# Kernel optimization log

Hardware: AMD Instinct MI355X
Metric: run time of the kernel (lower is better)

The kernel has to match this reference:

```python
import jax, jax.numpy as jnp
import numpy as np

B_SZ, C_IN, H, W = 2, 96, 128, 128
DT_RANK, D_STATE, D_INNER = 8, 16, 96


def pscan2d(A, X):
    """Faithful port of PScan2DUnified.forward / pscan2d_optimized.

    A, X: (b, H, W, d, N). The source's downsweep writes into index_select
    COPIES (discarded in torch), so the effective computation is the upsweep
    only: at level k (stride s=2**k), for each 2x2 block of active elements,
    X[dst] += A[dst] * X[src]; A[dst] *= A[src], where src=(s-1::2s, s-1::2s)
    and dst=(2s-1::2s, 2s-1::2s). Requires H, W powers of two.
    """
    h, w = A.shape[1], A.shape[2]
    K = min(int(np.log2(h)), int(np.log2(w)))
    for k in range(K):
        s = 2 ** k
        Asrc = A[:, s - 1::2 * s, s - 1::2 * s]
        Xsrc = X[:, s - 1::2 * s, s - 1::2 * s]
        Adst = A[:, 2 * s - 1::2 * s, 2 * s - 1::2 * s]
        X = X.at[:, 2 * s - 1::2 * s, 2 * s - 1::2 * s].add(Adst * Xsrc)
        A = A.at[:, 2 * s - 1::2 * s, 2 * s - 1::2 * s].multiply(Asrc)
    return X


def setup_inputs() -> dict:
    key = jax.random.key(0)
    ks = jax.random.split(key, 5)
    x = jax.random.normal(ks[0], (B_SZ, C_IN, H, W), dtype=jnp.float32)
    # 1x1 conv weights stored as (out, in) matrices
    deltaBC_w = jax.random.normal(ks[1], (DT_RANK + 2 * D_STATE, C_IN), dtype=jnp.float32) * 0.02
    deltaBC_b = jnp.zeros((DT_RANK + 2 * D_STATE,), dtype=jnp.float32)
    dt_w = jax.random.normal(ks[2], (D_INNER, DT_RANK), dtype=jnp.float32) * 0.02
    dt_b = jnp.zeros((D_INNER,), dtype=jnp.float32)
    # faithful init: log(linspace(1,2,N)) repeated over d_inner
    A_log = jnp.tile(jnp.log(jnp.linspace(1.0, 2.0, D_STATE, dtype=jnp.float32)), (D_INNER, 1))
    D = jnp.ones((D_INNER,), dtype=jnp.float32)
    return {"x": x, "deltaBC_w": deltaBC_w, "deltaBC_b": deltaBC_b,
            "dt_w": dt_w, "dt_b": dt_b, "A_log": A_log, "D": D}


def reference(x, deltaBC_w, deltaBC_b, dt_w, dt_b, A_log, D):
    A = -jnp.exp(A_log)  # (d, N)
    # 1x1 conv == per-pixel matmul
    dBC = jnp.einsum('bchw,oc->bohw', x, deltaBC_w) + deltaBC_b[None, :, None, None]
    delta = dBC[:, :DT_RANK]
    Bm = dBC[:, DT_RANK:DT_RANK + D_STATE]
    Cm = dBC[:, DT_RANK + D_STATE:]
    delta = jax.nn.softplus(jnp.einsum('bchw,oc->bohw', delta, dt_w) + dt_b[None, :, None, None])
    delta = delta.transpose(0, 2, 3, 1)   # (b,H,W,d)
    Bm = Bm.transpose(0, 2, 3, 1)         # (b,H,W,N)
    Cm = Cm.transpose(0, 2, 3, 1)         # (b,H,W,N)
    xh = x.transpose(0, 2, 3, 1)          # (b,H,W,d)
    A_bar = jnp.exp(delta[..., None] * A)                         # (b,H,W,d,N)
    BX = (delta[..., None] * Bm[:, :, :, None, :]) * xh[..., None]  # (b,H,W,d,N)
    hs = pscan2d(A_bar, BX)                                       # (b,H,W,d,N)
    y = jnp.einsum('bhwdn,bhwn->bhwd', hs, Cm) + D * xh
    return y
```

## Files before the change

### kernel.cpp

```cpp
#include <hip/hip_runtime.h>
#include <cstdint>

#define CIN 96
#define DIN 96
#define DTR 8
#define DST 16
#define HH 128
#define WW 128
#define HW (HH*WW)
#define NPIX (2*HW)
#define DIAG (WW+1)
#define SHORT_BLOCKS 2048
#define LONG_BLOCKS 512

__device__ __forceinline__ float softplus_f(float t) {
    return (t > 20.0f) ? t : __logf(1.0f + __expf(t));
}

__global__ __launch_bounds__(512) void ssm2d_dbc(
    const float* __restrict__ x,
    const float* __restrict__ W1, const float* __restrict__ b1,
    const float* __restrict__ dtw, const float* __restrict__ dtb,
    const float* __restrict__ alog, const float* __restrict__ Dv,
    float* __restrict__ bc, float2* __restrict__ dc,
    float* __restrict__ Aws, float* __restrict__ out)
{
    __shared__ float sX[CIN][65];
    __shared__ float sOut[64][41];
    __shared__ float sBC[64];

    const int t = threadIdx.x;
    const int p0 = blockIdx.x * 64;
    const int bb = p0 >> 14;
    const int q0 = p0 & (HW - 1);
    const float* xb = x + (size_t)bb * CIN * HW + q0;

    #pragma unroll
    for (int it = 0; it < 3; ++it) {
        int i = it * 512 + t;
        int ch = i >> 4;
        int p4 = (i & 15) << 2;
        float4 v = *reinterpret_cast<const float4*>(xb + (size_t)ch * HW + p4);
        sX[ch][p4 + 0] = v.x; sX[ch][p4 + 1] = v.y;
        sX[ch][p4 + 2] = v.z; sX[ch][p4 + 3] = v.w;
    }
    if (blockIdx.x == 0) {
        for (int i = t; i < DIN * DST; i += 512) {
            int d = i >> 4, n = i & 15;
            Aws[n * DIN + d] = -__expf(alog[i]);
        }
    }
    __syncthreads();

    const int lane = t & 63;
    const int w = __builtin_amdgcn_readfirstlane(t >> 6);
    const int og = w * 5;

    float a0 = b1[og + 0], a1 = b1[og + 1], a2 = b1[og + 2],
          a3 = b1[og + 3], a4 = b1[og + 4];
    #pragma unroll 16
    for (int ch = 0; ch < CIN; ++ch) {
        float xv = sX[ch][lane];
        a0 = fmaf(xv, W1[(og + 0) * CIN + ch], a0);
        a1 = fmaf(xv, W1[(og + 1) * CIN + ch], a1);
        a2 = fmaf(xv, W1[(og + 2) * CIN + ch], a2);
        a3 = fmaf(xv, W1[(og + 3) * CIN + ch], a3);
        a4 = fmaf(xv, W1[(og + 4) * CIN + ch], a4);
    }
    sOut[lane][og + 0] = a0; sOut[lane][og + 1] = a1; sOut[lane][og + 2] = a2;
    sOut[lane][og + 3] = a3; sOut[lane][og + 4] = a4;
    __syncthreads();

    if (t < 64) {
        float s = 0.f;
        #pragma unroll
        for (int n = 0; n < DST; ++n) s += sOut[t][8 + n] * sOut[t][24 + n];
        sBC[t] = s;
    }
    __syncthreads();

    #pragma unroll
    for (int it = 0; it < 12; ++it) {
        int i = it * 512 + t;
        int px = i / 96;
        int d = i - px * 96;
        float tt = dtb[d];
        float4 wA = *reinterpret_cast<const float4*>(dtw + d * DTR);
        float4 wB = *reinterpret_cast<const float4*>(dtw + d * DTR + 4);
        tt = fmaf(sOut[px][0], wA.x, tt); tt = fmaf(sOut[px][1], wA.y, tt);
        tt = fmaf(sOut[px][2], wA.z, tt); tt = fmaf(sOut[px][3], wA.w, tt);
        tt = fmaf(sOut[px][4], wB.x, tt); tt = fmaf(sOut[px][5], wB.y, tt);
        tt = fmaf(sOut[px][6], wB.z, tt); tt = fmaf(sOut[px][7], wB.w, tt);
        float delta = softplus_f(tt);
        float xv = sX[d][px];
        out[(size_t)p0 * 96 + i] = xv * fmaf(delta, sBC[px], Dv[d]);
        dc[(size_t)p0 * 96 + i] = make_float2(delta, delta * xv);
    }

    {
        int px = t >> 3;
        int o4 = (t & 7) << 2;
        float4 v = make_float4(sOut[px][8 + o4], sOut[px][9 + o4],
                               sOut[px][10 + o4], sOut[px][11 + o4]);
        *reinterpret_cast<float4*>(bc + (size_t)(p0 + px) * 32 + o4) = v;
    }
}

__global__ __launch_bounds__(384) void ssm2d_scan(
    const float* __restrict__ bc, const float2* __restrict__ dc,
    const float* __restrict__ Aws, float* __restrict__ out)
{
    const int t = threadIdx.x;
    if (blockIdx.x < SHORT_BLOCKS) {
        const int lp = t / DIN;
        const int d = t - lp * DIN;
        const int pix = blockIdx.x * 4 + lp;
        const int b = pix >> 12;
        const int rem = pix & 4095;
        const int r = ((rem >> 6) << 1) + 1;
        const int c = ((rem & 63) << 1) + 1;
        const int p = b * HW + r * WW + c;
        int m = __builtin_ctz(r + 1);
        int mc = __builtin_ctz(c + 1);
        if (mc < m) m = mc;
        if (m >= 5) return;
        const int L = 1 << m;

        float An[16];
        #pragma unroll
        for (int n = 0; n < 16; ++n) An[n] = Aws[n * DIN + d];
        float acc16[16];
        #pragma unroll
        for (int n = 0; n < 16; ++n) acc16[n] = 0.f;

        float S = dc[(size_t)p * 96 + d].x;
        int pj = p;
        for (int j = 1; j < L; ++j) {
            pj -= DIAG;
            float2 v = dc[(size_t)pj * 96 + d];
            float cj = v.y;
            const float* rb = bc + (size_t)pj * 32;
            float4 B0 = *reinterpret_cast<const float4*>(rb);
            float4 B1 = *reinterpret_cast<const float4*>(rb + 4);
            float4 B2 = *reinterpret_cast<const float4*>(rb + 8);
            float4 B3 = *reinterpret_cast<const float4*>(rb + 12);
            float Bv[16] = {B0.x,B0.y,B0.z,B0.w, B1.x,B1.y,B1.z,B1.w,
                            B2.x,B2.y,B2.z,B2.w, B3.x,B3.y,B3.z,B3.w};
            #pragma unroll
            for (int n = 0; n < 16; ++n)
                acc16[n] = fmaf(__expf(An[n] * S) * Bv[n], cj, acc16[n]);
            S += v.x;
        }
        const float* rc = bc + (size_t)p * 32 + 16;
        float4 C0 = *reinterpret_cast<const float4*>(rc);
        float4 C1 = *reinterpret_cast<const float4*>(rc + 4);
        float4 C2 = *reinterpret_cast<const float4*>(rc + 8);
        float4 C3 = *reinterpret_cast<const float4*>(rc + 12);
        float ys = 0.f;
        ys = fmaf(acc16[0],C0.x,ys); ys = fmaf(acc16[1],C0.y,ys);
        ys = fmaf(acc16[2],C0.z,ys); ys = fmaf(acc16[3],C0.w,ys);
        ys = fmaf(acc16[4],C1.x,ys); ys = fmaf(acc16[5],C1.y,ys);
        ys = fmaf(acc16[6],C1.z,ys); ys = fmaf(acc16[7],C1.w,ys);
        ys = fmaf(acc16[8],C2.x,ys); ys = fmaf(acc16[9],C2.y,ys);
        ys = fmaf(acc16[10],C2.z,ys); ys = fmaf(acc16[11],C2.w,ys);
        ys = fmaf(acc16[12],C3.x,ys); ys = fmaf(acc16[13],C3.y,ys);
        ys = fmaf(acc16[14],C3.z,ys); ys = fmaf(acc16[15],C3.w,ys);
        out[(size_t)p * 96 + d] += ys;
    } else {
        const int wv = t >> 6;
        const int lane = t & 63;
        int waveid = (blockIdx.x - SHORT_BLOCKS) * 6 + wv;
        int pix = waveid / DIN;
        int d = waveid - pix * DIN;
        int batch = pix >> 4;
        int sel = pix & 15;
        int r = ((sel >> 2) + 1) * 32 - 1;
        int c = ((sel & 3) + 1) * 32 - 1;
        int p = batch * HW + r * WW + c;
        int m = __builtin_ctz(r + 1);
        int mc = __builtin_ctz(c + 1);
        if (mc < m) m = mc;
        int L = 1 << m;

        float An[16];
        #pragma unroll
        for (int n = 0; n < 16; ++n) An[n] = Aws[n * DIN + d];

        float acc16[16];
        #pragma unroll
        for (int n = 0; n < 16; ++n) acc16[n] = 0.0f;
        float Scarry = 0.0f;

        for (int jb = 0; jb < L; jb += 64) {
            int j = jb + lane;
            bool act = (j < L);
            int jc = act ? j : 0;
            int pj = p - DIAG * jc;
            float2 v = dc[(size_t)pj * 96 + d];
            float dj = act ? v.x : 0.0f;
            float cj = (j >= 1 && act) ? v.y : 0.0f;

            float incl = dj;
            #pragma unroll
            for (int off = 1; off < 64; off <<= 1) {
                float u = __shfl_up(incl, off);
                if (lane >= off) incl += u;
            }
            float S = Scarry + incl - dj;

            const float* rb = bc + (size_t)pj * 32;
            float4 B0 = *reinterpret_cast<const float4*>(rb);
            float4 B1 = *reinterpret_cast<const float4*>(rb + 4);
            float4 B2 = *reinterpret_cast<const float4*>(rb + 8);
            float4 B3 = *reinterpret_cast<const float4*>(rb + 12);
            float Bv[16] = {B0.x,B0.y,B0.z,B0.w, B1.x,B1.y,B1.z,B1.w,
                            B2.x,B2.y,B2.z,B2.w, B3.x,B3.y,B3.z,B3.w};
            #pragma unroll
            for (int n = 0; n < 16; ++n)
                acc16[n] = fmaf(__expf(An[n] * S) * Bv[n], cj, acc16[n]);

            Scarry += __shfl(incl, 63);
        }

        #pragma unroll
        for (int off = 32; off >= 1; off >>= 1) {
            #pragma unroll
            for (int n = 0; n < 16; ++n) acc16[n] += __shfl_xor(acc16[n], off);
        }

        if (lane == 0) {
            const float* rc = bc + (size_t)p * 32 + 16;
            float4 C0 = *reinterpret_cast<const float4*>(rc);
            float4 C1 = *reinterpret_cast<const float4*>(rc + 4);
            float4 C2 = *reinterpret_cast<const float4*>(rc + 8);
            float4 C3 = *reinterpret_cast<const float4*>(rc + 12);
            float y = 0.0f;
            y = fmaf(acc16[0],C0.x,y); y = fmaf(acc16[1],C0.y,y);
            y = fmaf(acc16[2],C0.z,y); y = fmaf(acc16[3],C0.w,y);
            y = fmaf(acc16[4],C1.x,y); y = fmaf(acc16[5],C1.y,y);
            y = fmaf(acc16[6],C1.z,y); y = fmaf(acc16[7],C1.w,y);
            y = fmaf(acc16[8],C2.x,y); y = fmaf(acc16[9],C2.y,y);
            y = fmaf(acc16[10],C2.z,y); y = fmaf(acc16[11],C2.w,y);
            y = fmaf(acc16[12],C3.x,y); y = fmaf(acc16[13],C3.y,y);
            y = fmaf(acc16[14],C3.z,y); y = fmaf(acc16[15],C3.w,y);
            out[(size_t)p * 96 + d] += y;
        }
    }
}

extern "C" void kernel_launch(void* const* d_in, const int* in_sizes, int n_in,
                              void* d_out, int out_size, void* d_ws, size_t ws_size,
                              hipStream_t stream) {
    const float* x    = (const float*)d_in[0];
    const float* W1   = (const float*)d_in[1];
    const float* b1   = (const float*)d_in[2];
    const float* dtw  = (const float*)d_in[3];
    const float* dtb  = (const float*)d_in[4];
    const float* alog = (const float*)d_in[5];
    const float* Dv   = (const float*)d_in[6];
    float* out = (float*)d_out;

    char* ws = (char*)d_ws;
    float2* dc  = (float2*)(ws);
    float*  bcb = (float*)(ws + 25165824);
    float*  Aws = (float*)(ws + 29360128);

    hipLaunchKernelGGL(ssm2d_dbc, dim3(NPIX / 64), dim3(512), 0, stream,
                       x, W1, b1, dtw, dtb, alog, Dv,
                       bcb, dc, Aws, out);
    hipLaunchKernelGGL(ssm2d_scan, dim3(SHORT_BLOCKS + LONG_BLOCKS), dim3(384), 0, stream,
                       bcb, dc, Aws, out);
}
```

Before: 46.18 us.

## Split short scan chains into per-length block ranges with templated unrolled loops

The short-chain scan region is split into four block ranges, one per chain length (2, 4, 8, 16). Each block now handles only pixels of one length, which removes intra-block divergence and the early-exit threads, and the two shortest lengths use fully unrolled templated loops with loads issued up front. The A matrix is stored transposed (d-major) with log2(e) folded in, so it loads as float4s and exp2f replaces __expf. More blocks are launched, and the branch selection and index math grow slightly more complex.

```diff
diff --git a/kernel.cpp b/kernel.cpp
--- a/kernel.cpp
+++ b/kernel.cpp
@@ -10,11 +10,112 @@
 #define HW (HH*WW)
 #define NPIX (2*HW)
 #define DIAG (WW+1)
-#define SHORT_BLOCKS 2048
+#define LOG2E 1.4426950408889634f
+
+#define M1_BLOCKS 2048
+#define M2_BLOCKS 512
+#define M3_BLOCKS 128
+#define M4_BLOCKS 32
 #define LONG_BLOCKS 512
+#define SCAN_BLOCKS (M1_BLOCKS + M2_BLOCKS + M3_BLOCKS + M4_BLOCKS + LONG_BLOCKS)
 
 __device__ __forceinline__ float softplus_f(float t) {
     return (t > 20.0f) ? t : __logf(1.0f + __expf(t));
+}
+
+__device__ __forceinline__ void load_An(const float* __restrict__ AwsT, int d, float* An) {
+    float4 A0 = *reinterpret_cast<const float4*>(AwsT + d * 16);
+    float4 A1 = *reinterpret_cast<const float4*>(AwsT + d * 16 + 4);
+    float4 A2 = *reinterpret_cast<const float4*>(AwsT + d * 16 + 8);
+    float4 A3 = *reinterpret_cast<const float4*>(AwsT + d * 16 + 12);
+    An[0]=A0.x; An[1]=A0.y; An[2]=A0.z; An[3]=A0.w;
+    An[4]=A1.x; An[5]=A1.y; An[6]=A1.z; An[7]=A1.w;
+    An[8]=A2.x; An[9]=A2.y; An[10]=A2.z; An[11]=A2.w;
+    An[12]=A3.x; An[13]=A3.y; An[14]=A3.z; An[15]=A3.w;
+}
+
+__device__ __forceinline__ float c_dot(const float* __restrict__ rc, const float* acc16) {
+    float4 C0 = *reinterpret_cast<const float4*>(rc);
+    float4 C1 = *reinterpret_cast<const float4*>(rc + 4);
+    float4 C2 = *reinterpret_cast<const float4*>(rc + 8);
+    float4 C3 = *reinterpret_cast<const float4*>(rc + 12);
+    float ys = 0.f;
+    ys = fmaf(acc16[0],C0.x,ys); ys = fmaf(acc16[1],C0.y,ys);
+    ys = fmaf(acc16[2],C0.z,ys); ys = fmaf(acc16[3],C0.w,ys);
+    ys = fmaf(acc16[4],C1.x,ys); ys = fmaf(acc16[5],C1.y,ys);
+    ys = fmaf(acc16[6],C1.z,ys); ys = fmaf(acc16[7],C1.w,ys);
+    ys = fmaf(acc16[8],C2.x,ys); ys = fmaf(acc16[9],C2.y,ys);
+    ys = fmaf(acc16[10],C2.z,ys); ys = fmaf(acc16[11],C2.w,ys);
+    ys = fmaf(acc16[12],C3.x,ys); ys = fmaf(acc16[13],C3.y,ys);
+    ys = fmaf(acc16[14],C3.z,ys); ys = fmaf(acc16[15],C3.w,ys);
+    return ys;
+}
+
+template<int L>
+__device__ __forceinline__ void chain_LT(int p, int d,
+    const float* __restrict__ bc, const float2* __restrict__ dc,
+    const float* __restrict__ AwsT, float* __restrict__ out)
+{
+    size_t base = (size_t)p * 96 + d;
+    float ybase = out[base];
+    float2 v0 = dc[base];
+    float2 vj[L - 1];
+    #pragma unroll
+    for (int j = 1; j < L; ++j)
+        vj[j - 1] = dc[(size_t)(p - j * DIAG) * 96 + d];
+    float An[16];
+    load_An(AwsT, d, An);
+    float acc16[16];
+    #pragma unroll
+    for (int n = 0; n < 16; ++n) acc16[n] = 0.f;
+    float S = v0.x;
+    #pragma unroll
+    for (int j = 1; j < L; ++j) {
+        const float* rb = bc + (size_t)(p - j * DIAG) * 32;
+        float4 B0 = *reinterpret_cast<const float4*>(rb);
+        float4 B1 = *reinterpret_cast<const float4*>(rb + 4);
+        float4 B2 = *reinterpret_cast<const float4*>(rb + 8);
+        float4 B3 = *reinterpret_cast<const float4*>(rb + 12);
+        float Bv[16] = {B0.x,B0.y,B0.z,B0.w, B1.x,B1.y,B1.z,B1.w,
+                        B2.x,B2.y,B2.z,B2.w, B3.x,B3.y,B3.z,B3.w};
+        float cj = vj[j - 1].y;
+        #pragma unroll
+        for (int n = 0; n < 16; ++n)
+            acc16[n] = fmaf(exp2f(An[n] * S) * Bv[n], cj, acc16[n]);
+        S += vj[j - 1].x;
+    }
+    out[base] = ybase + c_dot(bc + (size_t)p * 32 + 16, acc16);
+}
+
+__device__ __forceinline__ void chain_RT(int p, int d, int L,
+    const float* __restrict__ bc, const float2* __restrict__ dc,
+    const float* __restrict__ AwsT, float* __restrict__ out)
+{
+    size_t base = (size_t)p * 96 + d;
+    float ybase = out[base];
+    float An[16];
+    load_An(AwsT, d, An);
+    float acc16[16];
+    #pragma unroll
+    for (int n = 0; n < 16; ++n) acc16[n] = 0.f;
+    float S = dc[base].x;
+    int pj = p;
+    for (int j = 1; j < L; ++j) {
+        pj -= DIAG;
+        float2 v = dc[(size_t)pj * 96 + d];
+        const float* rb = bc + (size_t)pj * 32;
+        float4 B0 = *reinterpret_cast<const float4*>(rb);
+        float4 B1 = *reinterpret_cast<const float4*>(rb + 4);
+        float4 B2 = *reinterpret_cast<const float4*>(rb + 8);
+        float4 B3 = *reinterpret_cast<const float4*>(rb + 12);
+        float Bv[16] = {B0.x,B0.y,B0.z,B0.w, B1.x,B1.y,B1.z,B1.w,
+                        B2.x,B2.y,B2.z,B2.w, B3.x,B3.y,B3.z,B3.w};
+        #pragma unroll
+        for (int n = 0; n < 16; ++n)
+            acc16[n] = fmaf(exp2f(An[n] * S) * Bv[n], v.y, acc16[n]);
+        S += v.x;
+    }
+    out[base] = ybase + c_dot(bc + (size_t)p * 32 + 16, acc16);
 }
 
 __global__ __launch_bounds__(512) void ssm2d_dbc(
@@ -45,10 +146,8 @@
         sX[ch][p4 + 2] = v.z; sX[ch][p4 + 3] = v.w;
     }
     if (blockIdx.x == 0) {
-        for (int i = t; i < DIN * DST; i += 512) {
-            int d = i >> 4, n = i & 15;
-            Aws[n * DIN + d] = -__expf(alog[i]);
-        }
+        for (int i = t; i < DIN * DST; i += 512)
+            Aws[i] = -__expf(alog[i]) * LOG2E;
     }
     __syncthreads();
 
@@ -108,68 +207,37 @@
 
 __global__ __launch_bounds__(384) void ssm2d_scan(
     const float* __restrict__ bc, const float2* __restrict__ dc,
-    const float* __restrict__ Aws, float* __restrict__ out)
+    const float* __restrict__ AwsT, float* __restrict__ out)
 {
     const int t = threadIdx.x;
-    if (blockIdx.x < SHORT_BLOCKS) {
+    const int blk = blockIdx.x;
+    if (blk < M1_BLOCKS + M2_BLOCKS + M3_BLOCKS + M4_BLOCKS) {
+        int M, base;
+        if (blk < M1_BLOCKS)                          { M = 1; base = 0; }
+        else if (blk < M1_BLOCKS + M2_BLOCKS)         { M = 2; base = M1_BLOCKS; }
+        else if (blk < M1_BLOCKS + M2_BLOCKS + M3_BLOCKS) { M = 3; base = M1_BLOCKS + M2_BLOCKS; }
+        else                                          { M = 4; base = M1_BLOCKS + M2_BLOCKS + M3_BLOCKS; }
         const int lp = t / DIN;
         const int d = t - lp * DIN;
-        const int pix = blockIdx.x * 4 + lp;
-        const int b = pix >> 12;
-        const int rem = pix & 4095;
-        const int r = ((rem >> 6) << 1) + 1;
-        const int c = ((rem & 63) << 1) + 1;
-        const int p = b * HW + r * WW + c;
-        int m = __builtin_ctz(r + 1);
-        int mc = __builtin_ctz(c + 1);
-        if (mc < m) m = mc;
-        if (m >= 5) return;
-        const int L = 1 << m;
-
-        float An[16];
-        #pragma unroll
-        for (int n = 0; n < 16; ++n) An[n] = Aws[n * DIN + d];
-        float acc16[16];
-        #pragma unroll
-        for (int n = 0; n < 16; ++n) acc16[n] = 0.f;
-
-        float S = dc[(size_t)p * 96 + d].x;
-        int pj = p;
-        for (int j = 1; j < L; ++j) {
-            pj -= DIAG;
-            float2 v = dc[(size_t)pj * 96 + d];
-            float cj = v.y;
-            const float* rb = bc + (size_t)pj * 32;
-            float4 B0 = *reinterpret_cast<const float4*>(rb);
-            float4 B1 = *reinterpret_cast<const float4*>(rb + 4);
-            float4 B2 = *reinterpret_cast<const float4*>(rb + 8);
-            float4 B3 = *reinterpret_cast<const float4*>(rb + 12);
-            float Bv[16] = {B0.x,B0.y,B0.z,B0.w, B1.x,B1.y,B1.z,B1.w,
-                            B2.x,B2.y,B2.z,B2.w, B3.x,B3.y,B3.z,B3.w};
-            #pragma unroll
-            for (int n = 0; n < 16; ++n)
-                acc16[n] = fmaf(__expf(An[n] * S) * Bv[n], cj, acc16[n]);
-            S += v.x;
-        }
-        const float* rc = bc + (size_t)p * 32 + 16;
-        float4 C0 = *reinterpret_cast<const float4*>(rc);
-        float4 C1 = *reinterpret_cast<const float4*>(rc + 4);
-        float4 C2 = *reinterpret_cast<const float4*>(rc + 8);
-        float4 C3 = *reinterpret_cast<const float4*>(rc + 12);
-        float ys = 0.f;
-        ys = fmaf(acc16[0],C0.x,ys); ys = fmaf(acc16[1],C0.y,ys);
-        ys = fmaf(acc16[2],C0.z,ys); ys = fmaf(acc16[3],C0.w,ys);
-        ys = fmaf(acc16[4],C1.x,ys); ys = fmaf(acc16[5],C1.y,ys);
-        ys = fmaf(acc16[6],C1.z,ys); ys = fmaf(acc16[7],C1.w,ys);
-        ys = fmaf(acc16[8],C2.x,ys); ys = fmaf(acc16[9],C2.y,ys);
-        ys = fmaf(acc16[10],C2.z,ys); ys = fmaf(acc16[11],C2.w,ys);
-        ys = fmaf(acc16[12],C3.x,ys); ys = fmaf(acc16[13],C3.y,ys);
-        ys = fmaf(acc16[14],C3.z,ys); ys = fmaf(acc16[15],C3.w,ys);
-        out[(size_t)p * 96 + d] += ys;
+        int idx = (blk - base) * 4 + lp;
+        int nM = 128 >> M;
+        int half = nM * nM;
+        int img = idx >= half;
+        int e = idx - img * half;
+        int rr = e >> (7 - M);
+        int cc = e & (nM - 1);
+        if (((rr & cc) & 1) != 0) return;
+        int r = ((rr + 1) << M) - 1;
+        int cx = ((cc + 1) << M) - 1;
+        int p = img * HW + r * WW + cx;
+        if (M == 1)      chain_LT<2>(p, d, bc, dc, AwsT, out);
+        else if (M == 2) chain_LT<4>(p, d, bc, dc, AwsT, out);
+        else if (M == 3) chain_RT(p, d, 8, bc, dc, AwsT, out);
+        else             chain_RT(p, d, 16, bc, dc, AwsT, out);
     } else {
         const int wv = t >> 6;
         const int lane = t & 63;
-        int waveid = (blockIdx.x - SHORT_BLOCKS) * 6 + wv;
+        int waveid = (blk - (M1_BLOCKS + M2_BLOCKS + M3_BLOCKS + M4_BLOCKS)) * 6 + wv;
         int pix = waveid / DIN;
         int d = waveid - pix * DIN;
         int batch = pix >> 4;
@@ -183,8 +251,7 @@
         int L = 1 << m;
 
         float An[16];
-        #pragma unroll
-        for (int n = 0; n < 16; ++n) An[n] = Aws[n * DIN + d];
+        load_An(AwsT, d, An);
 
         float acc16[16];
         #pragma unroll
@@ -217,7 +284,7 @@
                             B2.x,B2.y,B2.z,B2.w, B3.x,B3.y,B3.z,B3.w};
             #pragma unroll
             for (int n = 0; n < 16; ++n)
-                acc16[n] = fmaf(__expf(An[n] * S) * Bv[n], cj, acc16[n]);
+                acc16[n] = fmaf(exp2f(An[n] * S) * Bv[n], cj, acc16[n]);
 
             Scarry += __shfl(incl, 63);
         }
@@ -229,20 +296,7 @@
         }
 
         if (lane == 0) {
-            const float* rc = bc + (size_t)p * 32 + 16;
-            float4 C0 = *reinterpret_cast<const float4*>(rc);
-            float4 C1 = *reinterpret_cast<const float4*>(rc + 4);
-            float4 C2 = *reinterpret_cast<const float4*>(rc + 8);
-            float4 C3 = *reinterpret_cast<const float4*>(rc + 12);
-            float y = 0.0f;
-            y = fmaf(acc16[0],C0.x,y); y = fmaf(acc16[1],C0.y,y);
-            y = fmaf(acc16[2],C0.z,y); y = fmaf(acc16[3],C0.w,y);
-            y = fmaf(acc16[4],C1.x,y); y = fmaf(acc16[5],C1.y,y);
-            y = fmaf(acc16[6],C1.z,y); y = fmaf(acc16[7],C1.w,y);
-            y = fmaf(acc16[8],C2.x,y); y = fmaf(acc16[9],C2.y,y);
-            y = fmaf(acc16[10],C2.z,y); y = fmaf(acc16[11],C2.w,y);
-            y = fmaf(acc16[12],C3.x,y); y = fmaf(acc16[13],C3.y,y);
-            y = fmaf(acc16[14],C3.z,y); y = fmaf(acc16[15],C3.w,y);
+            float y = c_dot(bc + (size_t)p * 32 + 16, acc16);
             out[(size_t)p * 96 + d] += y;
         }
     }
@@ -268,6 +322,6 @@
     hipLaunchKernelGGL(ssm2d_dbc, dim3(NPIX / 64), dim3(512), 0, stream,
                        x, W1, b1, dtw, dtb, alog, Dv,
                        bcb, dc, Aws, out);
-    hipLaunchKernelGGL(ssm2d_scan, dim3(SHORT_BLOCKS + LONG_BLOCKS), dim3(384), 0, stream,
+    hipLaunchKernelGGL(ssm2d_scan, dim3(SCAN_BLOCKS), dim3(384), 0, stream,
                        bcb, dc, Aws, out);
 }
```

Measured after the change: 47.79 us. +3.5%, slower.

## Replace per-pixel scan with per-diagonal LDS-staged prefix-sum kernel

Applied to the files above, without the earlier changes.

The scan stage is restructured so each block handles one anti-diagonal of one batch. It stages delta (recomputed from stored dt-rank projections), delta*x, B and C into LDS, then builds prefix sums of delta along the diagonal so each segment sum becomes a difference of two prefix values. This removes the repeated global gathers and per-wave shuffle scans of the old short/long split, and halves the dc workspace by storing only delta*x plus the 8-wide rank vector. The exp is folded into exp2 with a pre-scaled A, laid out d-major for float4 loads. The new grid is only 254 blocks with heavy LDS use (~110KB per block) and uneven diagonal lengths, so occupancy and load balance become risks.

```diff
diff --git a/kernel.cpp b/kernel.cpp
--- a/kernel.cpp
+++ b/kernel.cpp
@@ -10,11 +10,21 @@
 #define HW (HH*WW)
 #define NPIX (2*HW)
 #define DIAG (WW+1)
-#define SHORT_BLOCKS 2048
-#define LONG_BLOCKS 512
+#define LOG2E 1.4426950408889634f
 
 __device__ __forceinline__ float softplus_f(float t) {
     return (t > 20.0f) ? t : __logf(1.0f + __expf(t));
+}
+
+__device__ __forceinline__ void load_An(const float* __restrict__ AwsT, int d, float* An) {
+    float4 A0 = *reinterpret_cast<const float4*>(AwsT + d * 16);
+    float4 A1 = *reinterpret_cast<const float4*>(AwsT + d * 16 + 4);
+    float4 A2 = *reinterpret_cast<const float4*>(AwsT + d * 16 + 8);
+    float4 A3 = *reinterpret_cast<const float4*>(AwsT + d * 16 + 12);
+    An[0]=A0.x; An[1]=A0.y; An[2]=A0.z; An[3]=A0.w;
+    An[4]=A1.x; An[5]=A1.y; An[6]=A1.z; An[7]=A1.w;
+    An[8]=A2.x; An[9]=A2.y; An[10]=A2.z; An[11]=A2.w;
+    An[12]=A3.x; An[13]=A3.y; An[14]=A3.z; An[15]=A3.w;
 }
 
 __global__ __launch_bounds__(512) void ssm2d_dbc(
@@ -22,7 +32,7 @@
     const float* __restrict__ W1, const float* __restrict__ b1,
     const float* __restrict__ dtw, const float* __restrict__ dtb,
     const float* __restrict__ alog, const float* __restrict__ Dv,
-    float* __restrict__ bc, float2* __restrict__ dc,
+    float* __restrict__ bc, float* __restrict__ cjb, float* __restrict__ kkb,
     float* __restrict__ Aws, float* __restrict__ out)
 {
     __shared__ float sX[CIN][65];
@@ -45,10 +55,8 @@
         sX[ch][p4 + 2] = v.z; sX[ch][p4 + 3] = v.w;
     }
     if (blockIdx.x == 0) {
-        for (int i = t; i < DIN * DST; i += 512) {
-            int d = i >> 4, n = i & 15;
-            Aws[n * DIN + d] = -__expf(alog[i]);
-        }
+        for (int i = t; i < DIN * DST; i += 512)
+            Aws[i] = -__expf(alog[i]) * LOG2E;
     }
     __syncthreads();
 
@@ -94,9 +102,14 @@
         float delta = softplus_f(tt);
         float xv = sX[d][px];
         out[(size_t)p0 * 96 + i] = xv * fmaf(delta, sBC[px], Dv[d]);
-        dc[(size_t)p0 * 96 + i] = make_float2(delta, delta * xv);
-    }
-
+        cjb[(size_t)p0 * 96 + i] = delta * xv;
+    }
+
+    {
+        int px = t >> 3;
+        int o = t & 7;
+        kkb[(size_t)(p0 + px) * 8 + o] = sOut[px][o];
+    }
     {
         int px = t >> 3;
         int o4 = (t & 7) << 2;
@@ -106,145 +119,110 @@
     }
 }
 
-__global__ __launch_bounds__(384) void ssm2d_scan(
-    const float* __restrict__ bc, const float2* __restrict__ dc,
+__global__ __launch_bounds__(512) void ssm2d_diag(
+    const float* __restrict__ cjb, const float* __restrict__ kkb,
+    const float* __restrict__ bcb,
+    const float* __restrict__ dtw, const float* __restrict__ dtb,
     const float* __restrict__ Aws, float* __restrict__ out)
 {
+    __shared__ float sP[128][96];
+    __shared__ float sCJ[128][96];
+    __shared__ float sB[128][16];
+    __shared__ float sC[128][16];
+    __shared__ float sTot[8][96];
+
     const int t = threadIdx.x;
-    if (blockIdx.x < SHORT_BLOCKS) {
-        const int lp = t / DIN;
-        const int d = t - lp * DIN;
-        const int pix = blockIdx.x * 4 + lp;
-        const int b = pix >> 12;
-        const int rem = pix & 4095;
-        const int r = ((rem >> 6) << 1) + 1;
-        const int c = ((rem & 63) << 1) + 1;
-        const int p = b * HW + r * WW + c;
-        int m = __builtin_ctz(r + 1);
-        int mc = __builtin_ctz(c + 1);
-        if (mc < m) m = mc;
-        if (m >= 5) return;
-        const int L = 1 << m;
-
-        float An[16];
-        #pragma unroll
-        for (int n = 0; n < 16; ++n) An[n] = Aws[n * DIN + d];
-        float acc16[16];
-        #pragma unroll
-        for (int n = 0; n < 16; ++n) acc16[n] = 0.f;
-
-        float S = dc[(size_t)p * 96 + d].x;
-        int pj = p;
-        for (int j = 1; j < L; ++j) {
-            pj -= DIAG;
-            float2 v = dc[(size_t)pj * 96 + d];
-            float cj = v.y;
-            const float* rb = bc + (size_t)pj * 32;
-            float4 B0 = *reinterpret_cast<const float4*>(rb);
-            float4 B1 = *reinterpret_cast<const float4*>(rb + 4);
-            float4 B2 = *reinterpret_cast<const float4*>(rb + 8);
-            float4 B3 = *reinterpret_cast<const float4*>(rb + 12);
-            float Bv[16] = {B0.x,B0.y,B0.z,B0.w, B1.x,B1.y,B1.z,B1.w,
-                            B2.x,B2.y,B2.z,B2.w, B3.x,B3.y,B3.z,B3.w};
-            #pragma unroll
-            for (int n = 0; n < 16; ++n)
-                acc16[n] = fmaf(__expf(An[n] * S) * Bv[n], cj, acc16[n]);
-            S += v.x;
+    const int blk = blockIdx.x;
+    const int b = (blk >= 127) ? 1 : 0;
+    const int kd = blk - b * 127;
+    const int k = 2 * kd + 1;
+    const int r0 = (k > 127) ? (k - 127) : 0;
+    const int c0 = (k < 127) ? (127 - k) : 0;
+    const int adiff = (k > 127) ? (k - 127) : (127 - k);
+    const int dlen = 128 - adiff;
+    const int p0 = b * HW + r0 * WW + c0;
+
+    for (int i = t; i < dlen * 96; i += 512) {
+        int j = i / 96;
+        int d = i - j * 96;
+        size_t pg = (size_t)(p0 + j * DIAG);
+        sCJ[j][d] = cjb[pg * 96 + d];
+        const float* kr = kkb + pg * 8;
+        float4 k0 = *reinterpret_cast<const float4*>(kr);
+        float4 k1 = *reinterpret_cast<const float4*>(kr + 4);
+        float4 wA = *reinterpret_cast<const float4*>(dtw + d * DTR);
+        float4 wB = *reinterpret_cast<const float4*>(dtw + d * DTR + 4);
+        float tt = dtb[d];
+        tt = fmaf(k0.x, wA.x, tt); tt = fmaf(k0.y, wA.y, tt);
+        tt = fmaf(k0.z, wA.z, tt); tt = fmaf(k0.w, wA.w, tt);
+        tt = fmaf(k1.x, wB.x, tt); tt = fmaf(k1.y, wB.y, tt);
+        tt = fmaf(k1.z, wB.z, tt); tt = fmaf(k1.w, wB.w, tt);
+        sP[j][d] = softplus_f(tt);
+    }
+    for (int i = t; i < dlen * 16; i += 512) {
+        int j = i >> 4;
+        int n = i & 15;
+        const float* rb = bcb + (size_t)(p0 + j * DIAG) * 32;
+        sB[j][n] = rb[n];
+        sC[j][n] = rb[16 + n];
+    }
+    __syncthreads();
+
+    const int nch = (dlen + 15) >> 4;
+    for (int i = t; i < nch * 96; i += 512) {
+        int ch = i / 96;
+        int d = i - ch * 96;
+        float run = 0.f;
+        int j0 = ch << 4;
+        int j1 = j0 + 16; if (j1 > dlen) j1 = dlen;
+        for (int j = j0; j < j1; ++j) { run += sP[j][d]; sP[j][d] = run; }
+        sTot[ch][d] = run;
+    }
+    __syncthreads();
+    if (t < 96) {
+        float run = 0.f;
+        for (int ch = 0; ch < nch; ++ch) {
+            float v = sTot[ch][t];
+            sTot[ch][t] = run;
+            run += v;
         }
-        const float* rc = bc + (size_t)p * 32 + 16;
-        float4 C0 = *reinterpret_cast<const float4*>(rc);
-        float4 C1 = *reinterpret_cast<const float4*>(rc + 4);
-        float4 C2 = *reinterpret_cast<const float4*>(rc + 8);
-        float4 C3 = *reinterpret_cast<const float4*>(rc + 12);
-        float ys = 0.f;
-        ys = fmaf(acc16[0],C0.x,ys); ys = fmaf(acc16[1],C0.y,ys);
-        ys = fmaf(acc16[2],C0.z,ys); ys = fmaf(acc16[3],C0.w,ys);
-        ys = fmaf(acc16[4],C1.x,ys); ys = fmaf(acc16[5],C1.y,ys);
-        ys = fmaf(acc16[6],C1.z,ys); ys = fmaf(acc16[7],C1.w,ys);
-        ys = fmaf(acc16[8],C2.x,ys); ys = fmaf(acc16[9],C2.y,ys);
-        ys = fmaf(acc16[10],C2.z,ys); ys = fmaf(acc16[11],C2.w,ys);
-        ys = fmaf(acc16[12],C3.x,ys); ys = fmaf(acc16[13],C3.y,ys);
-        ys = fmaf(acc16[14],C3.z,ys); ys = fmaf(acc16[15],C3.w,ys);
-        out[(size_t)p * 96 + d] += ys;
-    } else {
-        const int wv = t >> 6;
-        const int lane = t & 63;
-        int waveid = (blockIdx.x - SHORT_BLOCKS) * 6 + wv;
-        int pix = waveid / DIN;
-        int d = waveid - pix * DIN;
-        int batch = pix >> 4;
-        int sel = pix & 15;
-        int r = ((sel >> 2) + 1) * 32 - 1;
-        int c = ((sel & 3) + 1) * 32 - 1;
-        int p = batch * HW + r * WW + c;
+    }
+    __syncthreads();
+    for (int i = t; i < dlen * 96; i += 512) {
+        int j = i / 96;
+        int d = i - j * 96;
+        sP[j][d] += sTot[j >> 4][d];
+    }
+    __syncthreads();
+
+    for (int i = t; i < dlen * 96; i += 512) {
+        int j = i / 96;
+        int d = i - j * 96;
+        int r = r0 + j, c = c0 + j;
+        if (!((r & c) & 1)) continue;
         int m = __builtin_ctz(r + 1);
         int mc = __builtin_ctz(c + 1);
         if (mc < m) m = mc;
         int L = 1 << m;
 
         float An[16];
+        load_An(Aws, d, An);
+        float acc[16];
         #pragma unroll
-        for (int n = 0; n < 16; ++n) An[n] = Aws[n * DIN + d];
-
-        float acc16[16];
-        #pragma unroll
-        for (int n = 0; n < 16; ++n) acc16[n] = 0.0f;
-        float Scarry = 0.0f;
-
-        for (int jb = 0; jb < L; jb += 64) {
-            int j = jb + lane;
-            bool act = (j < L);
-            int jc = act ? j : 0;
-            int pj = p - DIAG * jc;
-            float2 v = dc[(size_t)pj * 96 + d];
-            float dj = act ? v.x : 0.0f;
-            float cj = (j >= 1 && act) ? v.y : 0.0f;
-
-            float incl = dj;
-            #pragma unroll
-            for (int off = 1; off < 64; off <<= 1) {
-                float u = __shfl_up(incl, off);
-                if (lane >= off) incl += u;
-            }
-            float S = Scarry + incl - dj;
-
-            const float* rb = bc + (size_t)pj * 32;
-            float4 B0 = *reinterpret_cast<const float4*>(rb);
-            float4 B1 = *reinterpret_cast<const float4*>(rb + 4);
-            float4 B2 = *reinterpret_cast<const float4*>(rb + 8);
-            float4 B3 = *reinterpret_cast<const float4*>(rb + 12);
-            float Bv[16] = {B0.x,B0.y,B0.z,B0.w, B1.x,B1.y,B1.z,B1.w,
-                            B2.x,B2.y,B2.z,B2.w, B3.x,B3.y,B3.z,B3.w};
+        for (int n = 0; n < 16; ++n) acc[n] = 0.f;
+        float Pj = sP[j][d];
+        for (int s = 1; s < L; ++s) {
+            int a = j - s;
+            float Sv = Pj - sP[a][d];
+            float ca = sCJ[a][d];
             #pragma unroll
             for (int n = 0; n < 16; ++n)
-                acc16[n] = fmaf(__expf(An[n] * S) * Bv[n], cj, acc16[n]);
-
-            Scarry += __shfl(incl, 63);
+                acc[n] = fmaf(exp2f(An[n] * Sv) * sB[a][n], ca, acc[n]);
         }
-
+        float y = 0.f;
         #pragma unroll
-        for (int off = 32; off >= 1; off >>= 1) {
-            #pragma unroll
-            for (int n = 0; n < 16; ++n) acc16[n] += __shfl_xor(acc16[n], off);
-        }
-
-        if (lane == 0) {
-            const float* rc = bc + (size_t)p * 32 + 16;
-            float4 C0 = *reinterpret_cast<const float4*>(rc);
-            float4 C1 = *reinterpret_cast<const float4*>(rc + 4);
-            float4 C2 = *reinterpret_cast<const float4*>(rc + 8);
-            float4 C3 = *reinterpret_cast<const float4*>(rc + 12);
-            float y = 0.0f;
-            y = fmaf(acc16[0],C0.x,y); y = fmaf(acc16[1],C0.y,y);
-            y = fmaf(acc16[2],C0.z,y); y = fmaf(acc16[3],C0.w,y);
-            y = fmaf(acc16[4],C1.x,y); y = fmaf(acc16[5],C1.y,y);
-            y = fmaf(acc16[6],C1.z,y); y = fmaf(acc16[7],C1.w,y);
-            y = fmaf(acc16[8],C2.x,y); y = fmaf(acc16[9],C2.y,y);
-            y = fmaf(acc16[10],C2.z,y); y = fmaf(acc16[11],C2.w,y);
-            y = fmaf(acc16[12],C3.x,y); y = fmaf(acc16[13],C3.y,y);
-            y = fmaf(acc16[14],C3.z,y); y = fmaf(acc16[15],C3.w,y);
-            out[(size_t)p * 96 + d] += y;
-        }
+        for (int n = 0; n < 16; ++n) y = fmaf(acc[n], sC[j][n], y);
+        out[(size_t)(p0 + j * DIAG) * 96 + d] += y;
     }
 }
 
@@ -261,13 +239,14 @@
     float* out = (float*)d_out;
 
     char* ws = (char*)d_ws;
-    float2* dc  = (float2*)(ws);
-    float*  bcb = (float*)(ws + 25165824);
-    float*  Aws = (float*)(ws + 29360128);
+    float* cjb = (float*)(ws);
+    float* kkb = (float*)(ws + 12582912);
+    float* bcb = (float*)(ws + 13631488);
+    float* Aws = (float*)(ws + 17825792);
 
     hipLaunchKernelGGL(ssm2d_dbc, dim3(NPIX / 64), dim3(512), 0, stream,
                        x, W1, b1, dtw, dtb, alog, Dv,
-                       bcb, dc, Aws, out);
-    hipLaunchKernelGGL(ssm2d_scan, dim3(SHORT_BLOCKS + LONG_BLOCKS), dim3(384), 0, stream,
-                       bcb, dc, Aws, out);
-}
+                       bcb, cjb, kkb, Aws, out);
+    hipLaunchKernelGGL(ssm2d_diag, dim3(254), dim3(512), 0, stream,
+                       cjb, kkb, bcb, dtw, dtb, Aws, out);
+}
```

Measured after the change: 160.2 us. +246.9%, slower.

## Fuse short-range diagonal scans into tiled projection kernel using shared memory

Applied to the files above, without the earlier changes.

The projection kernel now works on 8x8 spatial tiles and keeps delta, x, B and C in shared memory, so scan chains of length up to 8 are evaluated in the same kernel without going through global memory. Only pixels on every 16th diagonal have their delta and B/C written to the workspace, which the tail kernel needs for the length-16 and longer chains. The A coefficients are pre-scaled by log2(e) so the kernels can use exp2f. This trades more shared memory per block and a gathered, uncoalesced x load for far less workspace traffic and fewer scan threads in the second launch.

```diff
diff --git a/kernel.cpp b/kernel.cpp
--- a/kernel.cpp
+++ b/kernel.cpp
@@ -10,14 +10,13 @@
 #define HW (HH*WW)
 #define NPIX (2*HW)
 #define DIAG (WW+1)
-#define SHORT_BLOCKS 2048
-#define LONG_BLOCKS 512
+#define LOG2E 1.4426950408889634f
 
 __device__ __forceinline__ float softplus_f(float t) {
     return (t > 20.0f) ? t : __logf(1.0f + __expf(t));
 }
 
-__global__ __launch_bounds__(512) void ssm2d_dbc(
+__global__ __launch_bounds__(512) void ssm2d_tile(
     const float* __restrict__ x,
     const float* __restrict__ W1, const float* __restrict__ b1,
     const float* __restrict__ dtw, const float* __restrict__ dtb,
@@ -27,35 +26,35 @@
 {
     __shared__ float sX[CIN][65];
     __shared__ float sOut[64][41];
+    __shared__ float sDelta[DIN][65];
+    __shared__ float sAn[DIN][16];
     __shared__ float sBC[64];
 
     const int t = threadIdx.x;
-    const int p0 = blockIdx.x * 64;
-    const int bb = p0 >> 14;
-    const int q0 = p0 & (HW - 1);
-    const float* xb = x + (size_t)bb * CIN * HW + q0;
+    const int blk = blockIdx.x;
+    const int b = blk >> 8;
+    const int tile = blk & 255;
+    const int r0 = (tile >> 4) << 3;
+    const int c0 = (tile & 15) << 3;
+    const float* xb = x + (size_t)b * CIN * HW;
 
     #pragma unroll
-    for (int it = 0; it < 3; ++it) {
+    for (int it = 0; it < 12; ++it) {
         int i = it * 512 + t;
-        int ch = i >> 4;
-        int p4 = (i & 15) << 2;
-        float4 v = *reinterpret_cast<const float4*>(xb + (size_t)ch * HW + p4);
-        sX[ch][p4 + 0] = v.x; sX[ch][p4 + 1] = v.y;
-        sX[ch][p4 + 2] = v.z; sX[ch][p4 + 3] = v.w;
-    }
-    if (blockIdx.x == 0) {
-        for (int i = t; i < DIN * DST; i += 512) {
-            int d = i >> 4, n = i & 15;
-            Aws[n * DIN + d] = -__expf(alog[i]);
-        }
+        int ch = i >> 6;
+        int rel = i & 63;
+        sX[ch][rel] = xb[(size_t)ch * HW + (r0 + (rel >> 3)) * WW + (c0 + (rel & 7))];
+    }
+    for (int i = t; i < DIN * DST; i += 512) {
+        float v = -__expf(alog[i]) * LOG2E;
+        sAn[i >> 4][i & 15] = v;
+        if (blk == 0) Aws[i] = v;
     }
     __syncthreads();
 
     const int lane = t & 63;
     const int w = __builtin_amdgcn_readfirstlane(t >> 6);
     const int og = w * 5;
-
     float a0 = b1[og + 0], a1 = b1[og + 1], a2 = b1[og + 2],
           a3 = b1[og + 3], a4 = b1[og + 4];
     #pragma unroll 16
@@ -93,52 +92,100 @@
         tt = fmaf(sOut[px][6], wB.z, tt); tt = fmaf(sOut[px][7], wB.w, tt);
         float delta = softplus_f(tt);
         float xv = sX[d][px];
-        out[(size_t)p0 * 96 + i] = xv * fmaf(delta, sBC[px], Dv[d]);
-        dc[(size_t)p0 * 96 + i] = make_float2(delta, delta * xv);
-    }
-
-    {
-        int px = t >> 3;
-        int o4 = (t & 7) << 2;
-        float4 v = make_float4(sOut[px][8 + o4], sOut[px][9 + o4],
-                               sOut[px][10 + o4], sOut[px][11 + o4]);
-        *reinterpret_cast<float4*>(bc + (size_t)(p0 + px) * 32 + o4) = v;
+        sDelta[d][px] = delta;
+        int rg = r0 + (px >> 3), cg = c0 + (px & 7);
+        size_t pg = (size_t)b * HW + rg * WW + cg;
+        out[pg * 96 + d] = xv * fmaf(delta, sBC[px], Dv[d]);
+        if (((rg - cg) & 15) == 0)
+            dc[pg * 96 + d] = make_float2(delta, delta * xv);
+    }
+    #pragma unroll
+    for (int it = 0; it < 4; ++it) {
+        int i = it * 512 + t;
+        int px = i >> 5;
+        int n = i & 31;
+        int rg = r0 + (px >> 3), cg = c0 + (px & 7);
+        if (((rg - cg) & 15) == 0) {
+            size_t pg = (size_t)b * HW + rg * WW + cg;
+            bc[pg * 32 + n] = sOut[px][8 + n];
+        }
+    }
+    __syncthreads();
+
+    for (int ii = t; ii < 16 * 96; ii += 512) {
+        int oi = ii / 96;
+        int d = ii - oi * 96;
+        int i4 = oi >> 2, j4 = oi & 3;
+        int px = 16 * i4 + 2 * j4 + 9;
+        int rg = r0 + (px >> 3), cg = c0 + (px & 7);
+        int m = __builtin_ctz(rg + 1);
+        int mc = __builtin_ctz(cg + 1);
+        if (mc < m) m = mc;
+        if (m >= 4) continue;
+        int L = 1 << m;
+        float An[16];
+        #pragma unroll
+        for (int n = 0; n < 16; ++n) An[n] = sAn[d][n];
+        float acc[16];
+        #pragma unroll
+        for (int n = 0; n < 16; ++n) acc[n] = 0.f;
+        float S = sDelta[d][px];
+        for (int s = 1; s < L; ++s) {
+            int a = px - 9 * s;
+            float da = sDelta[d][a];
+            float ca = da * sX[d][a];
+            #pragma unroll
+            for (int n = 0; n < 16; ++n)
+                acc[n] = fmaf(exp2f(An[n] * S) * sOut[a][8 + n], ca, acc[n]);
+            S += da;
+        }
+        float y = 0.f;
+        #pragma unroll
+        for (int n = 0; n < 16; ++n) y = fmaf(acc[n], sOut[px][24 + n], y);
+        size_t g = ((size_t)b * HW + rg * WW + cg) * 96 + d;
+        out[g] += y;
     }
 }
 
-__global__ __launch_bounds__(384) void ssm2d_scan(
+__global__ __launch_bounds__(256) void ssm2d_tail(
     const float* __restrict__ bc, const float2* __restrict__ dc,
-    const float* __restrict__ Aws, float* __restrict__ out)
+    const float* __restrict__ AwsT, float* __restrict__ out)
 {
     const int t = threadIdx.x;
-    if (blockIdx.x < SHORT_BLOCKS) {
-        const int lp = t / DIN;
-        const int d = t - lp * DIN;
-        const int pix = blockIdx.x * 4 + lp;
-        const int b = pix >> 12;
-        const int rem = pix & 4095;
-        const int r = ((rem >> 6) << 1) + 1;
-        const int c = ((rem & 63) << 1) + 1;
-        const int p = b * HW + r * WW + c;
-        int m = __builtin_ctz(r + 1);
-        int mc = __builtin_ctz(c + 1);
-        if (mc < m) m = mc;
-        if (m >= 5) return;
-        const int L = 1 << m;
+    const int blk = blockIdx.x;
+
+    if (blk < 48) {
+        int e = blk * 256 + t;
+        int d = e % 96;
+        int pxi = e / 96;
+        int img = pxi >> 6;
+        int sel = pxi & 63;
+        int a = sel >> 3, b2 = sel & 7;
+        int r = a * 16 + 15, c = b2 * 16 + 15;
+        bool live = !((a & 1) && (b2 & 1));
+        int p = img * HW + r * WW + c;
+        size_t base = (size_t)p * 96 + d;
 
         float An[16];
-        #pragma unroll
-        for (int n = 0; n < 16; ++n) An[n] = Aws[n * DIN + d];
-        float acc16[16];
-        #pragma unroll
-        for (int n = 0; n < 16; ++n) acc16[n] = 0.f;
-
-        float S = dc[(size_t)p * 96 + d].x;
+        {
+            float4 A0 = *reinterpret_cast<const float4*>(AwsT + d * 16);
+            float4 A1 = *reinterpret_cast<const float4*>(AwsT + d * 16 + 4);
+            float4 A2 = *reinterpret_cast<const float4*>(AwsT + d * 16 + 8);
+            float4 A3 = *reinterpret_cast<const float4*>(AwsT + d * 16 + 12);
+            An[0]=A0.x; An[1]=A0.y; An[2]=A0.z; An[3]=A0.w;
+            An[4]=A1.x; An[5]=A1.y; An[6]=A1.z; An[7]=A1.w;
+            An[8]=A2.x; An[9]=A2.y; An[10]=A2.z; An[11]=A2.w;
+            An[12]=A3.x; An[13]=A3.y; An[14]=A3.z; An[15]=A3.w;
+        }
+        float acc[16];
+        #pragma unroll
+        for (int n = 0; n < 16; ++n) acc[n] = 0.f;
+        float S = dc[base].x;
         int pj = p;
-        for (int j = 1; j < L; ++j) {
+        #pragma unroll 4
+        for (int j = 1; j < 16; ++j) {
             pj -= DIAG;
             float2 v = dc[(size_t)pj * 96 + d];
-            float cj = v.y;
             const float* rb = bc + (size_t)pj * 32;
             float4 B0 = *reinterpret_cast<const float4*>(rb);
             float4 B1 = *reinterpret_cast<const float4*>(rb + 4);
@@ -148,7 +195,7 @@
                             B2.x,B2.y,B2.z,B2.w, B3.x,B3.y,B3.z,B3.w};
             #pragma unroll
             for (int n = 0; n < 16; ++n)
-                acc16[n] = fmaf(__expf(An[n] * S) * Bv[n], cj, acc16[n]);
+                acc[n] = fmaf(exp2f(An[n] * S) * Bv[n], v.y, acc[n]);
             S += v.x;
         }
         const float* rc = bc + (size_t)p * 32 + 16;
@@ -156,20 +203,20 @@
         float4 C1 = *reinterpret_cast<const float4*>(rc + 4);
         float4 C2 = *reinterpret_cast<const float4*>(rc + 8);
         float4 C3 = *reinterpret_cast<const float4*>(rc + 12);
-        float ys = 0.f;
-        ys = fmaf(acc16[0],C0.x,ys); ys = fmaf(acc16[1],C0.y,ys);
-        ys = fmaf(acc16[2],C0.z,ys); ys = fmaf(acc16[3],C0.w,ys);
-        ys = fmaf(acc16[4],C1.x,ys); ys = fmaf(acc16[5],C1.y,ys);
-        ys = fmaf(acc16[6],C1.z,ys); ys = fmaf(acc16[7],C1.w,ys);
-        ys = fmaf(acc16[8],C2.x,ys); ys = fmaf(acc16[9],C2.y,ys);
-        ys = fmaf(acc16[10],C2.z,ys); ys = fmaf(acc16[11],C2.w,ys);
-        ys = fmaf(acc16[12],C3.x,ys); ys = fmaf(acc16[13],C3.y,ys);
-        ys = fmaf(acc16[14],C3.z,ys); ys = fmaf(acc16[15],C3.w,ys);
-        out[(size_t)p * 96 + d] += ys;
+        float y = 0.f;
+        y = fmaf(acc[0],C0.x,y); y = fmaf(acc[1],C0.y,y);
+        y = fmaf(acc[2],C0.z,y); y = fmaf(acc[3],C0.w,y);
+        y = fmaf(acc[4],C1.x,y); y = fmaf(acc[5],C1.y,y);
+        y = fmaf(acc[6],C1.z,y); y = fmaf(acc[7],C1.w,y);
+        y = fmaf(acc[8],C2.x,y); y = fmaf(acc[9],C2.y,y);
+        y = fmaf(acc[10],C2.z,y); y = fmaf(acc[11],C2.w,y);
+        y = fmaf(acc[12],C3.x,y); y = fmaf(acc[13],C3.y,y);
+        y = fmaf(acc[14],C3.z,y); y = fmaf(acc[15],C3.w,y);
+        if (live) out[base] += y;
     } else {
         const int wv = t >> 6;
         const int lane = t & 63;
-        int waveid = (blockIdx.x - SHORT_BLOCKS) * 6 + wv;
+        int waveid = (blk - 48) * 4 + wv;
         int pix = waveid / DIN;
         int d = waveid - pix * DIN;
         int batch = pix >> 4;
@@ -183,12 +230,19 @@
         int L = 1 << m;
 
         float An[16];
-        #pragma unroll
-        for (int n = 0; n < 16; ++n) An[n] = Aws[n * DIN + d];
-
-        float acc16[16];
-        #pragma unroll
-        for (int n = 0; n < 16; ++n) acc16[n] = 0.0f;
+        {
+            float4 A0 = *reinterpret_cast<const float4*>(AwsT + d * 16);
+            float4 A1 = *reinterpret_cast<const float4*>(AwsT + d * 16 + 4);
+            float4 A2 = *reinterpret_cast<const float4*>(AwsT + d * 16 + 8);
+            float4 A3 = *reinterpret_cast<const float4*>(AwsT + d * 16 + 12);
+            An[0]=A0.x; An[1]=A0.y; An[2]=A0.z; An[3]=A0.w;
+            An[4]=A1.x; An[5]=A1.y; An[6]=A1.z; An[7]=A1.w;
+            An[8]=A2.x; An[9]=A2.y; An[10]=A2.z; An[11]=A2.w;
+            An[12]=A3.x; An[13]=A3.y; An[14]=A3.z; An[15]=A3.w;
+        }
+        float acc[16];
+        #pragma unroll
+        for (int n = 0; n < 16; ++n) acc[n] = 0.0f;
         float Scarry = 0.0f;
 
         for (int jb = 0; jb < L; jb += 64) {
@@ -217,7 +271,7 @@
                             B2.x,B2.y,B2.z,B2.w, B3.x,B3.y,B3.z,B3.w};
             #pragma unroll
             for (int n = 0; n < 16; ++n)
-                acc16[n] = fmaf(__expf(An[n] * S) * Bv[n], cj, acc16[n]);
+                acc[n] = fmaf(exp2f(An[n] * S) * Bv[n], cj, acc[n]);
 
             Scarry += __shfl(incl, 63);
         }
@@ -225,7 +279,7 @@
         #pragma unroll
         for (int off = 32; off >= 1; off >>= 1) {
             #pragma unroll
-            for (int n = 0; n < 16; ++n) acc16[n] += __shfl_xor(acc16[n], off);
+            for (int n = 0; n < 16; ++n) acc[n] += __shfl_xor(acc[n], off);
         }
 
         if (lane == 0) {
@@ -234,15 +288,15 @@
             float4 C1 = *reinterpret_cast<const float4*>(rc + 4);
             float4 C2 = *reinterpret_cast<const float4*>(rc + 8);
             float4 C3 = *reinterpret_cast<const float4*>(rc + 12);
-            float y = 0.0f;
-            y = fmaf(acc16[0],C0.x,y); y = fmaf(acc16[1],C0.y,y);
-            y = fmaf(acc16[2],C0.z,y); y = fmaf(acc16[3],C0.w,y);
-            y = fmaf(acc16[4],C1.x,y); y = fmaf(acc16[5],C1.y,y);
-            y = fmaf(acc16[6],C1.z,y); y = fmaf(acc16[7],C1.w,y);
-            y = fmaf(acc16[8],C2.x,y); y = fmaf(acc16[9],C2.y,y);
-            y = fmaf(acc16[10],C2.z,y); y = fmaf(acc16[11],C2.w,y);
-            y = fmaf(acc16[12],C3.x,y); y = fmaf(acc16[13],C3.y,y);
-            y = fmaf(acc16[14],C3.z,y); y = fmaf(acc16[15],C3.w,y);
+            float y = 0.f;
+            y = fmaf(acc[0],C0.x,y); y = fmaf(acc[1],C0.y,y);
+            y = fmaf(acc[2],C0.z,y); y = fmaf(acc[3],C0.w,y);
+            y = fmaf(acc[4],C1.x,y); y = fmaf(acc[5],C1.y,y);
+            y = fmaf(acc[6],C1.z,y); y = fmaf(acc[7],C1.w,y);
+            y = fmaf(acc[8],C2.x,y); y = fmaf(acc[9],C2.y,y);
+            y = fmaf(acc[10],C2.z,y); y = fmaf(acc[11],C2.w,y);
+            y = fmaf(acc[12],C3.x,y); y = fmaf(acc[13],C3.y,y);
+            y = fmaf(acc[14],C3.z,y); y = fmaf(acc[15],C3.w,y);
             out[(size_t)p * 96 + d] += y;
         }
     }
@@ -265,9 +319,9 @@
     float*  bcb = (float*)(ws + 25165824);
     float*  Aws = (float*)(ws + 29360128);
 
-    hipLaunchKernelGGL(ssm2d_dbc, dim3(NPIX / 64), dim3(512), 0, stream,
+    hipLaunchKernelGGL(ssm2d_tile, dim3(512), dim3(512), 0, stream,
                        x, W1, b1, dtw, dtb, alog, Dv,
                        bcb, dc, Aws, out);
-    hipLaunchKernelGGL(ssm2d_scan, dim3(SHORT_BLOCKS + LONG_BLOCKS), dim3(384), 0, stream,
+    hipLaunchKernelGGL(ssm2d_tail, dim3(48 + 768), dim3(256), 0, stream,
                        bcb, dc, Aws, out);
 }
```

Result: slower. 47.28 us (+2.4%).
